# Performance work log

Measured on AMD Instinct MI355X. Metric: run time of the kernel, lower is better.

Reference implementation:

```python
import jax, jax.numpy as jnp
import numpy as np

BIG = 1.0e8  # masked_fill value from the torch module


def setup_inputs() -> dict:
    key = jax.random.key(0)
    k1, k2, k3, k4 = jax.random.split(key, 4)
    B, N, M, D = 32, 2048, 2048, 3
    o_weights = jax.random.randint(k1, (B, N), 0, 2, dtype=jnp.int32)
    outputs = jax.random.normal(k2, (B, N, D), dtype=jnp.float32)
    t_weights = jax.random.randint(k3, (B, M), 0, 2, dtype=jnp.int32)
    targets = jax.random.normal(k4, (B, M, D), dtype=jnp.float32)
    return {"o_weights": o_weights, "outputs": outputs, "t_weights": t_weights, "targets": targets}


def _chamfer(mask_a, pc_a, mask_b, pc_b):
    # pairwise Euclidean distances [B, N, M] via ||a||^2 + ||b||^2 - 2 a.b
    a2 = jnp.sum(pc_a * pc_a, axis=-1)  # [B, N]
    b2 = jnp.sum(pc_b * pc_b, axis=-1)  # [B, M]
    ab = jnp.einsum("bnd,bmd->bnm", pc_a, pc_b)
    d2 = jnp.maximum(a2[..., :, None] + b2[..., None, :] - 2.0 * ab, 0.0)
    dist = jnp.sqrt(d2)  # [B, N, M]
    mm = (mask_a != 0)[..., :, None] & (mask_b != 0)[..., None, :]
    dist = jnp.where(mm, dist, BIG)
    ma = mask_a.astype(pc_a.dtype)
    mb = mask_b.astype(pc_b.dtype)
    min1 = jnp.min(dist, axis=-1) ** 2 * ma  # [B, N]
    min2 = jnp.min(dist, axis=-2) ** 2 * mb  # [B, M]
    return 0.5 * (jnp.sum(min1, axis=-1) + jnp.sum(min2, axis=-1))  # [B]


def reference(o_weights, outputs, t_weights, targets):
    return _chamfer(o_weights, outputs, t_weights, targets)
```

## Files before the change

### kernel.cpp

```cpp
#include <hip/hip_runtime.h>
#include <hip/hip_bf16.h>

#define B_    32
#define N_    2048
#define M_    2048
#define RW_   8
#define GX_   32
#define BIG2  1.0e16f

typedef float v2f __attribute__((ext_vector_type(2)));

__device__ __forceinline__ v2f v2_fma(v2f a, v2f b, v2f c) {
#if __has_builtin(__builtin_elementwise_fma)
    return __builtin_elementwise_fma(a, b, c);
#else
    v2f r; r.x = fmaf(a.x, b.x, c.x); r.y = fmaf(a.y, b.y, c.y); return r;
#endif
}
__device__ __forceinline__ v2f v2_min(v2f a, v2f b) {
#if __has_builtin(__builtin_elementwise_min)
    return __builtin_elementwise_min(a, b);
#else
    v2f r; r.x = fminf(a.x, b.x); r.y = fminf(a.y, b.y); return r;
#endif
}
__device__ __forceinline__ v2f v2_splat(float s) { return (v2f){ s, s }; }

union F4V2 { float4 f4; struct { v2f lo, hi; } v; };

__global__ __launch_bounds__(512) void chamfer_main(
    const int* __restrict__ o_w, const float* __restrict__ o_pts,
    const int* __restrict__ t_w, const float* __restrict__ t_pts,
    float* __restrict__ partials)
{
    const int dir  = blockIdx.z;
    const int b    = blockIdx.y;
    const int tid  = threadIdx.x;
    const int lane = tid & 63;
    const int wv   = tid >> 6;
    const int row0 = blockIdx.x * (8 * RW_) + wv * RW_;

    const int*   wa; const float* pa;
    const int*   wb; const float* pb;
    if (dir == 0) { wa = o_w; pa = o_pts; wb = t_w; pb = t_pts; }
    else          { wa = t_w; pa = t_pts; wb = o_w; pb = o_pts; }

    __shared__ float4 sqA[M_ / 2];
    __shared__ float4 sqB[M_ / 2];
    __shared__ float  wsum[8];

    {
        const float2* src2 = (const float2*)(pb + (size_t)b * M_ * 3);
        const int2*   wb2  = (const int2*)(wb + (size_t)b * M_);
        #pragma unroll
        for (int k = 0; k < 2; ++k) {
            int p = tid + k * 512;
            float2 u0 = src2[p * 3 + 0];
            float2 u1 = src2[p * 3 + 1];
            float2 u2 = src2[p * 3 + 2];
            int2   mm = wb2[p];
            float x0 = u0.x, y0 = u0.y, z0 = u1.x;
            float x1 = u1.y, y1 = u2.x, z1 = u2.y;
            float n20 = fmaf(x0, x0, fmaf(y0, y0, z0 * z0));
            float n21 = fmaf(x1, x1, fmaf(y1, y1, z1 * z1));
            sqA[p] = make_float4(-2.f * x0, -2.f * x1, -2.f * y0, -2.f * y1);
            sqB[p] = make_float4(-2.f * z0, -2.f * z1,
                                 mm.x ? n20 : BIG2, mm.y ? n21 : BIG2);
        }
    }

    int base = __builtin_amdgcn_readfirstlane((b * N_ + row0) * 3);
    const float* rp = pa + base;
    float rx[RW_], ry[RW_], rz[RW_];
    #pragma unroll
    for (int r = 0; r < RW_; ++r) {
        rx[r] = rp[3 * r + 0];
        ry[r] = rp[3 * r + 1];
        rz[r] = rp[3 * r + 2];
    }
    __syncthreads();

    v2f acc[RW_];
    #pragma unroll
    for (int r = 0; r < RW_; ++r) acc[r] = v2_splat(3.4e38f);

    F4V2 qa, qb, na, nb;
    qa.f4 = sqA[lane];
    qb.f4 = sqB[lane];
    #pragma unroll 4
    for (int t = 0; t < M_ / 128; ++t) {
        if (t + 1 < M_ / 128) {
            na.f4 = sqA[(t + 1) * 64 + lane];
            nb.f4 = sqB[(t + 1) * 64 + lane];
        }
        v2f xs = qa.v.lo, ys = qa.v.hi, zs = qb.v.lo, ws = qb.v.hi;
        #pragma unroll
        for (int r = 0; r < RW_; ++r) {
            v2f d = v2_fma(v2_splat(rx[r]), xs,
                    v2_fma(v2_splat(ry[r]), ys,
                    v2_fma(v2_splat(rz[r]), zs, ws)));
            acc[r] = v2_min(acc[r], d);
        }
        qa = na; qb = nb;
    }

    int mbase = __builtin_amdgcn_readfirstlane(b * N_ + row0);
    const int* wp = wa + mbase;
    float sum = 0.0f;
    #pragma unroll
    for (int r = 0; r < RW_; ++r) {
        float m = fminf(acc[r].x, acc[r].y);
        #pragma unroll
        for (int off = 32; off; off >>= 1)
            m = fminf(m, __shfl_xor(m, off, 64));
        float a2 = fmaf(rx[r], rx[r], fmaf(ry[r], ry[r], rz[r] * rz[r]));
        float d2 = fmaxf(a2 + m, 0.0f);
        sum += (wp[r] != 0) ? d2 : 0.0f;
    }
    if (lane == 0) wsum[wv] = sum;
    __syncthreads();
    if (tid == 0) {
        float s = 0.f;
        #pragma unroll
        for (int i = 0; i < 8; ++i) s += wsum[i];
        partials[((size_t)b * 2 + dir) * GX_ + blockIdx.x] = s;
    }
}

__global__ __launch_bounds__(256) void chamfer_finish(
    const float* __restrict__ partials, float* __restrict__ loss)
{
    int t = threadIdx.x;
    int b = t >> 3, k = t & 7;
    const float4* p4 = (const float4*)(partials + b * (2 * GX_) + k * 8);
    float4 u = p4[0], v = p4[1];
    float s = ((u.x + u.y) + (u.z + u.w)) + ((v.x + v.y) + (v.z + v.w));
    #pragma unroll
    for (int off = 4; off; off >>= 1) s += __shfl_xor(s, off, 64);
    if (k == 0) loss[b] = 0.5f * s;
}

__global__ void chamfer_zero(float* __restrict__ loss)
{
    if (threadIdx.x < B_) loss[threadIdx.x] = 0.0f;
}

__global__ __launch_bounds__(256) void chamfer_nolds(
    const int* __restrict__ o_w, const float* __restrict__ o_pts,
    const int* __restrict__ t_w, const float* __restrict__ t_pts,
    float* __restrict__ loss)
{
    const int dir  = blockIdx.z;
    const int b    = blockIdx.y;
    const int lane = threadIdx.x & 63;
    const int wv   = threadIdx.x >> 6;
    const int row0 = (blockIdx.x * 4 + wv) * 16;

    const int*   __restrict__ wa = (dir == 0) ? o_w   : t_w;
    const float* __restrict__ pa = (dir == 0) ? o_pts : t_pts;
    const int*   __restrict__ wb = (dir == 0) ? t_w   : o_w;
    const float* __restrict__ pb = (dir == 0) ? t_pts : o_pts;

    int base = __builtin_amdgcn_readfirstlane((b * N_ + row0) * 3);
    const float* rp = pa + base;
    float rx[16], ry[16], rz[16];
    #pragma unroll
    for (int r = 0; r < 16; ++r) {
        rx[r] = rp[3 * r + 0];
        ry[r] = rp[3 * r + 1];
        rz[r] = rp[3 * r + 2];
    }
    float acc[16];
    #pragma unroll
    for (int r = 0; r < 16; ++r) acc[r] = 3.4e38f;

    #pragma unroll 2
    for (int t = 0; t < M_ / 64; ++t) {
        int ib = b * M_ + t * 64 + lane;
        float bx = pb[ib * 3 + 0], by = pb[ib * 3 + 1], bz = pb[ib * 3 + 2];
        float n2 = fmaf(bx, bx, fmaf(by, by, bz * bz));
        float qw = (wb[ib] != 0) ? n2 : BIG2;
        float qx = -2.0f * bx, qy = -2.0f * by, qz = -2.0f * bz;
        #pragma unroll
        for (int r = 0; r < 16; ++r) {
            float d = fmaf(rx[r], qx, fmaf(ry[r], qy, fmaf(rz[r], qz, qw)));
            acc[r] = fminf(acc[r], d);
        }
    }
    #pragma unroll
    for (int r = 0; r < 16; ++r) {
        float v = acc[r];
        #pragma unroll
        for (int off = 32; off; off >>= 1) v = fminf(v, __shfl_xor(v, off, 64));
        acc[r] = v;
    }
    int mbase = __builtin_amdgcn_readfirstlane(b * N_ + row0);
    const int* wp = wa + mbase;
    float sum = 0.0f;
    #pragma unroll
    for (int r = 0; r < 16; ++r) {
        float a2 = fmaf(rx[r], rx[r], fmaf(ry[r], ry[r], rz[r] * rz[r]));
        float d2 = fmaxf(a2 + acc[r], 0.0f);
        sum += (wp[r] != 0) ? d2 : 0.0f;
    }
    if (lane == 0) atomicAdd(&loss[b], 0.5f * sum);
}

extern "C" void kernel_launch(void* const* d_in, const int* in_sizes, int n_in,
                              void* d_out, int out_size, void* d_ws, size_t ws_size,
                              hipStream_t stream) {
    const int*   o_w   = (const int*)  d_in[0];
    const float* o_pts = (const float*)d_in[1];
    const int*   t_w   = (const int*)  d_in[2];
    const float* t_pts = (const float*)d_in[3];
    float* loss = (float*)d_out;

    const size_t part_bytes = (size_t)B_ * 2 * GX_ * sizeof(float);

    if (ws_size >= part_bytes) {
        float* partials = (float*)d_ws;
        dim3 grid(GX_, B_, 2);
        chamfer_main<<<grid, 512, 0, stream>>>(
            o_w, o_pts, t_w, t_pts, partials);
        chamfer_finish<<<1, 256, 0, stream>>>(partials, loss);
    } else {
        chamfer_zero<<<1, 64, 0, stream>>>(loss);
        dim3 grid(N_ / 64, B_, 2);
        chamfer_nolds<<<grid, 256, 0, stream>>>(
            o_w, o_pts, t_w, t_pts, loss);
    }
}
```

Before: 85.65 us.

## Fuse both chamfer directions into one pass with row and column minima

Instead of launching separate blocks for each direction, each block now computes the masked squared-distance tile once. It keeps running minima both per row (outputs→targets) and per column (targets→outputs). Row-side norms and masks are folded into the distance term, so masked rows and columns are pushed out by a large constant. Per-chunk column minima are reduced in LDS and written to a workspace, and a new finish kernel reduces across chunks and adds the masked column sums. This halves the pairwise work in exchange for an extra add and min per pair, more registers, and an extra global write and read of column partials.

```diff
diff --git a/kernel.cpp b/kernel.cpp
--- a/kernel.cpp
+++ b/kernel.cpp
@@ -1,12 +1,12 @@
 #include <hip/hip_runtime.h>
-#include <hip/hip_bf16.h>
 
 #define B_    32
 #define N_    2048
 #define M_    2048
 #define RW_   8
-#define GX_   32
+#define CH_   32
 #define BIG2  1.0e16f
+#define FINF  3.4e38f
 
 typedef float v2f __attribute__((ext_vector_type(2)));
 
@@ -28,30 +28,28 @@
 
 union F4V2 { float4 f4; struct { v2f lo, hi; } v; };
 
-__global__ __launch_bounds__(512) void chamfer_main(
+__global__ __launch_bounds__(512) void chamfer_fused(
     const int* __restrict__ o_w, const float* __restrict__ o_pts,
     const int* __restrict__ t_w, const float* __restrict__ t_pts,
-    float* __restrict__ partials)
-{
-    const int dir  = blockIdx.z;
-    const int b    = blockIdx.y;
-    const int tid  = threadIdx.x;
-    const int lane = tid & 63;
-    const int wv   = tid >> 6;
-    const int row0 = blockIdx.x * (8 * RW_) + wv * RW_;
-
-    const int*   wa; const float* pa;
-    const int*   wb; const float* pb;
-    if (dir == 0) { wa = o_w; pa = o_pts; wb = t_w; pb = t_pts; }
-    else          { wa = t_w; pa = t_pts; wb = o_w; pb = o_pts; }
-
-    __shared__ float4 sqA[M_ / 2];
-    __shared__ float4 sqB[M_ / 2];
+    float* __restrict__ rowpart,
+    float* __restrict__ colpart)
+{
+    const int b     = blockIdx.y;
+    const int chunk = blockIdx.x;
+    const int tid   = threadIdx.x;
+    const int lane  = tid & 63;
+    const int wv    = tid >> 6;
+    const int row0  = chunk * (8 * RW_) + wv * RW_;
+
+    __shared__ float4 sq[2048];
     __shared__ float  wsum[8];
+    float4* sqA = sq;
+    float4* sqB = sq + 1024;
+    float*  colbuf = (float*)sq;
 
     {
-        const float2* src2 = (const float2*)(pb + (size_t)b * M_ * 3);
-        const int2*   wb2  = (const int2*)(wb + (size_t)b * M_);
+        const float2* src2 = (const float2*)(t_pts + (size_t)b * M_ * 3);
+        const int2*   wb2  = (const int2*)(t_w + (size_t)b * M_);
         #pragma unroll
         for (int k = 0; k < 2; ++k) {
             int p = tid + k * 512;
@@ -69,75 +67,140 @@
         }
     }
 
-    int base = __builtin_amdgcn_readfirstlane((b * N_ + row0) * 3);
-    const float* rp = pa + base;
-    float rx[RW_], ry[RW_], rz[RW_];
+    int base  = __builtin_amdgcn_readfirstlane((b * N_ + row0) * 3);
+    int mbase = __builtin_amdgcn_readfirstlane(b * N_ + row0);
+    const float* rp = o_pts + base;
+    const int*   wp = o_w + mbase;
+    float rx[RW_], ry[RW_], rz[RW_], ca2[RW_];
+    int   msk[RW_];
     #pragma unroll
     for (int r = 0; r < RW_; ++r) {
         rx[r] = rp[3 * r + 0];
         ry[r] = rp[3 * r + 1];
         rz[r] = rp[3 * r + 2];
-    }
-    __syncthreads();
-
-    v2f acc[RW_];
-    #pragma unroll
-    for (int r = 0; r < RW_; ++r) acc[r] = v2_splat(3.4e38f);
+        msk[r] = wp[r];
+        float a2 = fmaf(rx[r], rx[r], fmaf(ry[r], ry[r], rz[r] * rz[r]));
+        ca2[r] = msk[r] ? a2 : BIG2;
+    }
+    __syncthreads();
+
+    v2f racc[RW_];
+    v2f cacc[16];
+    #pragma unroll
+    for (int r = 0; r < RW_; ++r) racc[r] = v2_splat(FINF);
+    #pragma unroll
+    for (int t = 0; t < 16; ++t) cacc[t] = v2_splat(FINF);
 
     F4V2 qa, qb, na, nb;
     qa.f4 = sqA[lane];
     qb.f4 = sqB[lane];
-    #pragma unroll 4
-    for (int t = 0; t < M_ / 128; ++t) {
-        if (t + 1 < M_ / 128) {
+    #pragma unroll
+    for (int t = 0; t < 16; ++t) {
+        if (t + 1 < 16) {
             na.f4 = sqA[(t + 1) * 64 + lane];
             nb.f4 = sqB[(t + 1) * 64 + lane];
         }
         v2f xs = qa.v.lo, ys = qa.v.hi, zs = qb.v.lo, ws = qb.v.hi;
         #pragma unroll
         for (int r = 0; r < RW_; ++r) {
-            v2f d = v2_fma(v2_splat(rx[r]), xs,
-                    v2_fma(v2_splat(ry[r]), ys,
-                    v2_fma(v2_splat(rz[r]), zs, ws)));
-            acc[r] = v2_min(acc[r], d);
+            v2f wr = ws + v2_splat(ca2[r]);
+            v2f d  = v2_fma(v2_splat(rx[r]), xs,
+                     v2_fma(v2_splat(ry[r]), ys,
+                     v2_fma(v2_splat(rz[r]), zs, wr)));
+            racc[r] = v2_min(racc[r], d);
+            cacc[t] = v2_min(cacc[t], d);
         }
         qa = na; qb = nb;
     }
 
-    int mbase = __builtin_amdgcn_readfirstlane(b * N_ + row0);
-    const int* wp = wa + mbase;
     float sum = 0.0f;
     #pragma unroll
     for (int r = 0; r < RW_; ++r) {
-        float m = fminf(acc[r].x, acc[r].y);
+        float m = fminf(racc[r].x, racc[r].y);
         #pragma unroll
         for (int off = 32; off; off >>= 1)
             m = fminf(m, __shfl_xor(m, off, 64));
-        float a2 = fmaf(rx[r], rx[r], fmaf(ry[r], ry[r], rz[r] * rz[r]));
-        float d2 = fmaxf(a2 + m, 0.0f);
-        sum += (wp[r] != 0) ? d2 : 0.0f;
+        sum += msk[r] ? fmaxf(m, 0.0f) : 0.0f;
     }
     if (lane == 0) wsum[wv] = sum;
-    __syncthreads();
+
+    __syncthreads();
+
+    if (wv >= 4) {
+        #pragma unroll
+        for (int t = 0; t < 16; ++t)
+            *(v2f*)&colbuf[(wv - 4) * 2048 + t * 128 + 2 * lane] = cacc[t];
+    }
+    __syncthreads();
+    if (wv < 4) {
+        #pragma unroll
+        for (int t = 0; t < 16; ++t) {
+            v2f* p = (v2f*)&colbuf[wv * 2048 + t * 128 + 2 * lane];
+            *p = v2_min(*p, cacc[t]);
+        }
+    }
     if (tid == 0) {
         float s = 0.f;
         #pragma unroll
         for (int i = 0; i < 8; ++i) s += wsum[i];
-        partials[((size_t)b * 2 + dir) * GX_ + blockIdx.x] = s;
-    }
-}
-
-__global__ __launch_bounds__(256) void chamfer_finish(
-    const float* __restrict__ partials, float* __restrict__ loss)
-{
-    int t = threadIdx.x;
-    int b = t >> 3, k = t & 7;
-    const float4* p4 = (const float4*)(partials + b * (2 * GX_) + k * 8);
-    float4 u = p4[0], v = p4[1];
-    float s = ((u.x + u.y) + (u.z + u.w)) + ((v.x + v.y) + (v.z + v.w));
-    #pragma unroll
-    for (int off = 4; off; off >>= 1) s += __shfl_xor(s, off, 64);
-    if (k == 0) loss[b] = 0.5f * s;
+        rowpart[b * CH_ + chunk] = s;
+    }
+    __syncthreads();
+    if (wv < 2) {
+        #pragma unroll
+        for (int t = 0; t < 16; ++t) {
+            int c = t * 128 + 2 * lane;
+            v2f a  = *(v2f*)&colbuf[wv * 2048 + c];
+            v2f bb = *(v2f*)&colbuf[(wv + 2) * 2048 + c];
+            *(v2f*)&colbuf[wv * 2048 + c] = v2_min(a, bb);
+        }
+    }
+    __syncthreads();
+    {
+        float4 a  = *(float4*)&colbuf[0 * 2048 + tid * 4];
+        float4 bb = *(float4*)&colbuf[1 * 2048 + tid * 4];
+        float4 mn;
+        mn.x = fminf(a.x, bb.x);
+        mn.y = fminf(a.y, bb.y);
+        mn.z = fminf(a.z, bb.z);
+        mn.w = fminf(a.w, bb.w);
+        *(float4*)&colpart[((size_t)b * CH_ + chunk) * M_ + tid * 4] = mn;
+    }
+}
+
+__global__ __launch_bounds__(512) void chamfer_finish2(
+    const float* __restrict__ rowpart, const float* __restrict__ colpart,
+    const int* __restrict__ t_w, float* __restrict__ loss)
+{
+    const int b = blockIdx.x, tid = threadIdx.x;
+    const int lane = tid & 63, wv = tid >> 6;
+    const float4* cp = (const float4*)(colpart + (size_t)b * CH_ * M_);
+    float4 mn = cp[tid];
+    #pragma unroll 8
+    for (int k = 1; k < CH_; ++k) {
+        float4 v = cp[k * 512 + tid];
+        mn.x = fminf(mn.x, v.x);
+        mn.y = fminf(mn.y, v.y);
+        mn.z = fminf(mn.z, v.z);
+        mn.w = fminf(mn.w, v.w);
+    }
+    int4 mm = ((const int4*)(t_w + (size_t)b * M_))[tid];
+    float s = (mm.x ? fmaxf(mn.x, 0.f) : 0.f)
+            + (mm.y ? fmaxf(mn.y, 0.f) : 0.f)
+            + (mm.z ? fmaxf(mn.z, 0.f) : 0.f)
+            + (mm.w ? fmaxf(mn.w, 0.f) : 0.f);
+    if (tid < CH_) s += rowpart[b * CH_ + tid];
+    #pragma unroll
+    for (int off = 32; off; off >>= 1) s += __shfl_xor(s, off, 64);
+    __shared__ float ws8[8];
+    if (lane == 0) ws8[wv] = s;
+    __syncthreads();
+    if (tid == 0) {
+        float tot = 0.f;
+        #pragma unroll
+        for (int i = 0; i < 8; ++i) tot += ws8[i];
+        loss[b] = 0.5f * tot;
+    }
 }
 
 __global__ void chamfer_zero(float* __restrict__ loss)
@@ -215,14 +278,16 @@
     const float* t_pts = (const float*)d_in[3];
     float* loss = (float*)d_out;
 
-    const size_t part_bytes = (size_t)B_ * 2 * GX_ * sizeof(float);
-
-    if (ws_size >= part_bytes) {
-        float* partials = (float*)d_ws;
-        dim3 grid(GX_, B_, 2);
-        chamfer_main<<<grid, 512, 0, stream>>>(
-            o_w, o_pts, t_w, t_pts, partials);
-        chamfer_finish<<<1, 256, 0, stream>>>(partials, loss);
+    const size_t row_bytes = (size_t)B_ * CH_ * sizeof(float);
+    const size_t col_bytes = (size_t)B_ * CH_ * M_ * sizeof(float);
+
+    if (ws_size >= row_bytes + col_bytes) {
+        float* rowpart = (float*)d_ws;
+        float* colpart = (float*)d_ws + B_ * CH_;
+        dim3 grid(CH_, B_);
+        chamfer_fused<<<grid, 512, 0, stream>>>(
+            o_w, o_pts, t_w, t_pts, rowpart, colpart);
+        chamfer_finish2<<<B_, 512, 0, stream>>>(rowpart, colpart, t_w, loss);
     } else {
         chamfer_zero<<<1, 64, 0, stream>>>(loss);
         dim3 grid(N_ / 64, B_, 2);
```

Result: slower. 127.4 us (+48.7%).
